# Kernel optimization log

Measured on AMD Instinct MI355X. Metric: run time of the kernel, lower is better.

Reference implementation:

```python
import jax, jax.numpy as jnp
import numpy as np

N = 163842   # icosahedron level-7 vertices
CH = 64
EPS = 1e-5
SLOPE = 0.2

def _bn_lrelu(x, g, b):
    # BatchNorm1d over vertex dim (training-mode batch stats, biased var) + LeakyReLU(0.2)
    mu = jnp.mean(x, axis=0)
    var = jnp.var(x, axis=0)
    y = (x - mu) * jax.lax.rsqrt(var + EPS) * g + b
    return jnp.where(y > 0, y, SLOPE * y)

def _onering_conv(x, neigh, W, bias):
    # gather 7 one-ring neighbors per vertex, flatten, linear project
    n = x.shape[0]
    feat = x[neigh].reshape(n, -1)          # [N, 7*C]
    return feat @ W + bias                  # [N, out]

def setup_inputs() -> dict:
    key = jax.random.key(0)
    ks = jax.random.split(key, 8)
    d = {
        "x": jax.random.normal(ks[0], (N, CH), jnp.float32),
        "neigh_orders": jax.random.randint(ks[1], (7 * N,), 0, N, jnp.int64),
    }
    for i, k in enumerate([1, 2, 3, 4]):
        cin = CH * k
        d[f"g{k}"] = jnp.ones((cin,), jnp.float32)
        d[f"b{k}"] = jnp.zeros((cin,), jnp.float32)
        d[f"W{k}"] = jax.random.normal(ks[2 + i], (7 * cin, CH), jnp.float32) * (1.0 / np.sqrt(7 * cin))
        d[f"wb{k}"] = jnp.zeros((CH,), jnp.float32)
    return d

def reference(x, neigh_orders, g1, b1, g2, b2, g3, b3, g4, b4,
              W1, wb1, W2, wb2, W3, wb3, W4, wb4):
    x1 = _onering_conv(_bn_lrelu(x, g1, b1), neigh_orders, W1, wb1)
    c2 = jnp.concatenate((x, x1), axis=1)
    x2 = _onering_conv(_bn_lrelu(c2, g2, b2), neigh_orders, W2, wb2)
    c3 = jnp.concatenate((x, x1, x2), axis=1)
    x3 = _onering_conv(_bn_lrelu(c3, g3, b3), neigh_orders, W3, wb3)
    c4 = jnp.concatenate((x, x1, x2, x3), axis=1)
    x4 = _onering_conv(_bn_lrelu(c4, g4, b4), neigh_orders, W4, wb4)
    return x4
```

## Files before the change

kernel.cpp:

```cpp
#include <hip/hip_runtime.h>
#include <stdint.h>

#define NV 163842
#define EPSV 1e-5f

using short8 = __attribute__((ext_vector_type(8))) short;
using f32x4  = __attribute__((ext_vector_type(4))) float;

static __device__ __forceinline__ unsigned short f2bf(float f) {
    union { float f; unsigned int i; } v; v.f = f;
    return (unsigned short)((v.i + 0x7FFFu + ((v.i >> 16) & 1u)) >> 16);
}
static __device__ __forceinline__ void bf2x(unsigned int w, float& a, float& b) {
    union { unsigned int i; float f; } lo, hi;
    lo.i = w << 16; hi.i = w & 0xFFFF0000u;
    a = lo.f; b = hi.f;
}
static __device__ __forceinline__ unsigned int pack2(float a, float b) {
    union { float f; unsigned int i; } ua, ub; ua.f = a; ub.f = b;
    return __builtin_amdgcn_perm(ub.i + 0x8000u, ua.i + 0x8000u, 0x07060302);
}

__global__ __launch_bounds__(256) void k_zero(float* __restrict__ ACC) {
    ACC[threadIdx.x] = 0.f;
    ACC[256 + threadIdx.x] = 0.f;
}

__global__ __launch_bounds__(256) void k_cast(const float* __restrict__ x,
                                              unsigned short* __restrict__ C,
                                              float* __restrict__ ACC) {
    const int t = threadIdx.x;
    const int wv = t >> 6, lane = t & 63;
    const int v = blockIdx.x * 64 + (t >> 2);
    const int c0 = (t & 3) * 16;
    float f[16];
    const bool valid = v < NV;
    if (valid) {
        const float4* p = (const float4*)(x + (size_t)v * 64 + c0);
#pragma unroll
        for (int i = 0; i < 4; ++i) {
            float4 q = p[i];
            f[i * 4 + 0] = q.x; f[i * 4 + 1] = q.y; f[i * 4 + 2] = q.z; f[i * 4 + 3] = q.w;
        }
        unsigned int o[8];
#pragma unroll
        for (int i = 0; i < 8; ++i)
            o[i] = ((unsigned int)f2bf(f[2 * i])) | (((unsigned int)f2bf(f[2 * i + 1])) << 16);
        uint4* dst = (uint4*)(C + (size_t)v * 256 + c0);
        dst[0] = uint4{o[0], o[1], o[2], o[3]};
        dst[1] = uint4{o[4], o[5], o[6], o[7]};
    } else {
#pragma unroll
        for (int i = 0; i < 16; ++i) f[i] = 0.f;
    }
    float s[16], s2[16];
#pragma unroll
    for (int i = 0; i < 16; ++i) { s[i] = f[i]; s2[i] = f[i] * f[i]; }
#pragma unroll
    for (int mask = 4; mask <= 32; mask <<= 1) {
#pragma unroll
        for (int i = 0; i < 16; ++i) {
            s[i]  += __shfl_xor(s[i],  mask);
            s2[i] += __shfl_xor(s2[i], mask);
        }
    }
    __shared__ float red[4 * 128];
    if ((lane >> 2) == 0) {
        int cb = (lane & 3) * 16;
#pragma unroll
        for (int i = 0; i < 16; ++i) {
            red[wv * 128 + cb + i]      = s[i];
            red[wv * 128 + 64 + cb + i] = s2[i];
        }
    }
    __syncthreads();
    if (t < 128) {
        float v4 = red[t] + red[128 + t] + red[256 + t] + red[384 + t];
        int c = t & 63, which = t >> 6;
        atomicAdd(&ACC[which * 256 + c], v4);
    }
}

__global__ __launch_bounds__(256) void k_wt_all(const float* __restrict__ W1,
                                                const float* __restrict__ W2,
                                                const float* __restrict__ W3,
                                                const float* __restrict__ W4,
                                                unsigned short* __restrict__ WT) {
    int j = blockIdx.x * 256 + threadIdx.x;
    if (j >= 286720) return;
    const float* W; int jj, K7;
    if (j < 28672)       { W = W1; jj = j;          K7 = 448;  }
    else if (j < 86016)  { W = W2; jj = j - 28672;  K7 = 896;  }
    else if (j < 172032) { W = W3; jj = j - 86016;  K7 = 1344; }
    else                 { W = W4; jj = j - 172032; K7 = 1792; }
    int n = jj / K7, k = jj - n * K7;
    WT[j] = f2bf(W[(size_t)k * 64 + n]);
}

template<int CIN, int GRP, bool FINAL>
__global__ __launch_bounds__(256) void k_gg(const unsigned short* __restrict__ C,
                                            const int* __restrict__ neigh,
                                            const unsigned short* __restrict__ WT,
                                            const float* __restrict__ g,
                                            const float* __restrict__ bglob,
                                            const float* __restrict__ wb,
                                            float* __restrict__ ACC,
                                            unsigned short* __restrict__ Cout,
                                            float* __restrict__ Fout) {
    constexpr int KB = CIN / 64;
    constexpr int NC = 7 * KB;
    constexpr int K7 = 7 * CIN;

    __shared__ float ssc[256], ssh[256];
    __shared__ int sIdx[896];
    __shared__ unsigned short sA[128 * 72];
    __shared__ unsigned short sW[64 * 72];

    const int t = threadIdx.x;
    const int v0 = blockIdx.x * 128;

    if (t < CIN) {
        float s = ACC[t], s2 = ACC[256 + t];
        float mu = s * (1.0f / NV);
        float var = fmaf(-mu, mu, s2 * (1.0f / NV));
        float sc = g[t] * rsqrtf(var + EPSV);
        ssc[t] = sc;
        ssh[t] = bglob[t] - mu * sc;
    }
    for (int q = t; q < 896; q += 256) {
        int gi = v0 * 7 + q;
        sIdx[q] = (gi < NV * 7) ? neigh[gi] : 0;
    }
    __syncthreads();

    const int wv = t >> 6, lane = t & 63;
    const int m = lane & 15, quad = lane >> 4;
    const int arow = t >> 1, ahalf = t & 1;
    const int wrow = t >> 2, wq = t & 3;

    f32x4 acc[2][4];
#pragma unroll
    for (int i = 0; i < 2; ++i)
#pragma unroll
        for (int j = 0; j < 4; ++j) acc[i][j] = f32x4{0.f, 0.f, 0.f, 0.f};

    auto load_chunk = [&](int c, uint4* aa, uint4& x0, uint4& x1) {
        int r = c / KB, kb = c - r * KB;
        int src = sIdx[arow * 7 + r];
        const uint4* pa = (const uint4*)(C + (size_t)src * 256 + kb * 64 + ahalf * 32);
        aa[0] = pa[0]; aa[1] = pa[1]; aa[2] = pa[2]; aa[3] = pa[3];
        const uint4* pw = (const uint4*)(WT + (size_t)wrow * K7 + c * 64 + wq * 16);
        x0 = pw[0]; x1 = pw[1];
    };
    auto stage = [&](const uint4* aa, uint4 x0, uint4 x1, int c) {
        int kb = c - (c / KB) * KB;
        int chb = kb * 64 + ahalf * 32;
        unsigned short* dstA = sA + arow * 72 + ahalf * 32;
#pragma unroll
        for (int i = 0; i < 4; ++i) {
            unsigned int u[4] = {aa[i].x, aa[i].y, aa[i].z, aa[i].w};
            unsigned int o[4];
#pragma unroll
            for (int jj = 0; jj < 4; ++jj) {
                float lo, hi; bf2x(u[jj], lo, hi);
                int ch = chb + i * 8 + jj * 2;
                float y0 = fmaf(lo, ssc[ch],     ssh[ch]);
                float y1 = fmaf(hi, ssc[ch + 1], ssh[ch + 1]);
                y0 = y0 > 0.f ? y0 : 0.2f * y0;
                y1 = y1 > 0.f ? y1 : 0.2f * y1;
                o[jj] = pack2(y0, y1);
            }
            *(uint4*)(dstA + i * 8) = uint4{o[0], o[1], o[2], o[3]};
        }
        *(uint4*)(sW + wrow * 72 + wq * 16)     = x0;
        *(uint4*)(sW + wrow * 72 + wq * 16 + 8) = x1;
    };

    uint4 a[4], w0, w1;
    load_chunk(0, a, w0, w1);
#pragma unroll 2
    for (int c = 0; c < NC; ++c) {
        uint4 na[4], nw0, nw1;
        if (c + 1 < NC) load_chunk(c + 1, na, nw0, nw1);
        stage(a, w0, w1, c);
        __syncthreads();
#pragma unroll
        for (int s = 0; s < 2; ++s) {
            short8 af0 = *(const short8*)(sA + (wv * 32 + m) * 72      + s * 32 + quad * 8);
            short8 af1 = *(const short8*)(sA + (wv * 32 + 16 + m) * 72 + s * 32 + quad * 8);
#pragma unroll
            for (int ct = 0; ct < 4; ++ct) {
                short8 bf = *(const short8*)(sW + (ct * 16 + m) * 72 + s * 32 + quad * 8);
                acc[0][ct] = __builtin_amdgcn_mfma_f32_16x16x32_bf16(af0, bf, acc[0][ct], 0, 0, 0);
                acc[1][ct] = __builtin_amdgcn_mfma_f32_16x16x32_bf16(af1, bf, acc[1][ct], 0, 0, 0);
            }
        }
        __syncthreads();
        if (c + 1 < NC) {
#pragma unroll
            for (int i = 0; i < 4; ++i) a[i] = na[i];
            w0 = nw0; w1 = nw1;
        }
    }

    float bsum[4]  = {0.f, 0.f, 0.f, 0.f};
    float b2sum[4] = {0.f, 0.f, 0.f, 0.f};
#pragma unroll
    for (int mt = 0; mt < 2; ++mt) {
#pragma unroll
        for (int ct = 0; ct < 4; ++ct) {
            int col = ct * 16 + m;
            float bv = wb[col];
#pragma unroll
            for (int j = 0; j < 4; ++j) {
                int vr = v0 + wv * 32 + mt * 16 + quad * 4 + j;
                float val = acc[mt][ct][j] + bv;
                if (vr < NV) {
                    if (FINAL) {
                        Fout[(size_t)vr * 64 + col] = val;
                    } else {
                        Cout[(size_t)vr * 256 + GRP * 64 + col] = f2bf(val);
                        bsum[ct] += val; b2sum[ct] += val * val;
                    }
                }
            }
        }
    }
    if (!FINAL) {
#pragma unroll
        for (int ct = 0; ct < 4; ++ct) {
            bsum[ct]  += __shfl_xor(bsum[ct], 16);
            bsum[ct]  += __shfl_xor(bsum[ct], 32);
            b2sum[ct] += __shfl_xor(b2sum[ct], 16);
            b2sum[ct] += __shfl_xor(b2sum[ct], 32);
        }
        float* red = (float*)sA;
        if (quad == 0) {
#pragma unroll
            for (int ct = 0; ct < 4; ++ct) {
                red[wv * 128 + ct * 16 + m]       = bsum[ct];
                red[512 + wv * 128 + ct * 16 + m] = b2sum[ct];
            }
        }
        __syncthreads();
        if (t < 128) {
            int c = t & 63, which = t >> 6;
            float v = red[which * 512 + c] + red[which * 512 + 128 + c] +
                      red[which * 512 + 256 + c] + red[which * 512 + 384 + c];
            atomicAdd(&ACC[which * 256 + GRP * 64 + c], v);
        }
    }
}

extern "C" void kernel_launch(void* const* d_in, const int* in_sizes, int n_in,
                              void* d_out, int out_size, void* d_ws, size_t ws_size,
                              hipStream_t stream) {
    const float* x     = (const float*)d_in[0];
    const int*   neigh = (const int*)d_in[1];
    const float* G[4]  = {(const float*)d_in[2],  (const float*)d_in[6],
                          (const float*)d_in[10], (const float*)d_in[14]};
    const float* B[4]  = {(const float*)d_in[3],  (const float*)d_in[7],
                          (const float*)d_in[11], (const float*)d_in[15]};
    const float* W[4]  = {(const float*)d_in[4],  (const float*)d_in[8],
                          (const float*)d_in[12], (const float*)d_in[16]};
    const float* WB[4] = {(const float*)d_in[5],  (const float*)d_in[9],
                          (const float*)d_in[13], (const float*)d_in[17]};
    float* out = (float*)d_out;

    char* ws = (char*)d_ws;
    size_t off = 0;
    unsigned short* C  = (unsigned short*)(ws + off); off += (size_t)NV * 256 * 2;
    unsigned short* WT = (unsigned short*)(ws + off); off += (size_t)286720 * 2;
    float* ACC         = (float*)(ws + off);          off += 512 * 4;

    k_zero<<<1, 256, 0, stream>>>(ACC);
    k_cast<<<(NV + 63) / 64, 256, 0, stream>>>(x, C, ACC);
    k_wt_all<<<(286720 + 255) / 256, 256, 0, stream>>>(W[0], W[1], W[2], W[3], WT);

    const int GG = (NV + 127) / 128;
    k_gg< 64, 1, false><<<GG, 256, 0, stream>>>(C, neigh, WT,          G[0], B[0], WB[0], ACC, C, nullptr);
    k_gg<128, 2, false><<<GG, 256, 0, stream>>>(C, neigh, WT + 28672,  G[1], B[1], WB[1], ACC, C, nullptr);
    k_gg<192, 3, false><<<GG, 256, 0, stream>>>(C, neigh, WT + 86016,  G[2], B[2], WB[2], ACC, C, nullptr);
    k_gg<256, 0, true ><<<GG, 256, 0, stream>>>(C, neigh, WT + 172032, G[3], B[3], WB[3], ACC, nullptr, out);
}
```

Before: 528.0 us.

## Precompute BN+LeakyReLU activations and gather MFMA operands directly from global

Moves the BN+LeakyReLU normalisation out of the gather-GEMM into a separate per-layer elementwise pass that writes a compact activation buffer. The GEMM kernel then loads A fragments straight from global memory into registers with a 3-deep prefetch, skipping the LDS staging of A. Weights are staged into LDS in large segments of 14 chunks, so there are far fewer barriers. Blocks grow to 512 threads covering 256 vertices. The cost is an extra full read and write of the activations per layer, plus uncoalesced 16-byte gathers per lane.

```diff
diff --git a/kernel.cpp b/kernel.cpp
--- a/kernel.cpp
+++ b/kernel.cpp
@@ -97,28 +97,14 @@
     WT[j] = f2bf(W[(size_t)k * 64 + n]);
 }
 
-template<int CIN, int GRP, bool FINAL>
-__global__ __launch_bounds__(256) void k_gg(const unsigned short* __restrict__ C,
-                                            const int* __restrict__ neigh,
-                                            const unsigned short* __restrict__ WT,
-                                            const float* __restrict__ g,
-                                            const float* __restrict__ bglob,
-                                            const float* __restrict__ wb,
-                                            float* __restrict__ ACC,
-                                            unsigned short* __restrict__ Cout,
-                                            float* __restrict__ Fout) {
-    constexpr int KB = CIN / 64;
-    constexpr int NC = 7 * KB;
-    constexpr int K7 = 7 * CIN;
-
-    __shared__ float ssc[256], ssh[256];
-    __shared__ int sIdx[896];
-    __shared__ unsigned short sA[128 * 72];
-    __shared__ unsigned short sW[64 * 72];
-
+template<int CIN>
+__global__ __launch_bounds__(256) void k_apply(const unsigned short* __restrict__ C,
+                                               const float* __restrict__ ACC,
+                                               const float* __restrict__ g,
+                                               const float* __restrict__ bglob,
+                                               unsigned short* __restrict__ Y) {
+    __shared__ float ssc[CIN], ssh[CIN];
     const int t = threadIdx.x;
-    const int v0 = blockIdx.x * 128;
-
     if (t < CIN) {
         float s = ACC[t], s2 = ACC[256 + t];
         float mu = s * (1.0f / NV);
@@ -127,7 +113,48 @@
         ssc[t] = sc;
         ssh[t] = bglob[t] - mu * sc;
     }
-    for (int q = t; q < 896; q += 256) {
+    __syncthreads();
+    constexpr int C8 = CIN / 8;
+    int e = blockIdx.x * 256 + t;
+    if (e >= NV * C8) return;
+    int v = e / C8, c8 = e - v * C8;
+    int ch = c8 * 8;
+    uint4 u = *(const uint4*)(C + (size_t)v * 256 + ch);
+    float f[8];
+    bf2x(u.x, f[0], f[1]); bf2x(u.y, f[2], f[3]);
+    bf2x(u.z, f[4], f[5]); bf2x(u.w, f[6], f[7]);
+    unsigned int o[4];
+#pragma unroll
+    for (int jj = 0; jj < 4; ++jj) {
+        float y0 = fmaf(f[2 * jj],     ssc[ch + 2 * jj],     ssh[ch + 2 * jj]);
+        float y1 = fmaf(f[2 * jj + 1], ssc[ch + 2 * jj + 1], ssh[ch + 2 * jj + 1]);
+        y0 = y0 > 0.f ? y0 : 0.2f * y0;
+        y1 = y1 > 0.f ? y1 : 0.2f * y1;
+        o[jj] = pack2(y0, y1);
+    }
+    *(uint4*)(Y + (size_t)v * CIN + ch) = uint4{o[0], o[1], o[2], o[3]};
+}
+
+template<int CIN, int GRP, bool FINAL>
+__global__ __launch_bounds__(512, 4) void k_gg(const unsigned short* __restrict__ Y,
+                                               const int* __restrict__ neigh,
+                                               const unsigned short* __restrict__ WT,
+                                               const float* __restrict__ wb,
+                                               float* __restrict__ ACC,
+                                               unsigned short* __restrict__ Cout,
+                                               float* __restrict__ Fout) {
+    constexpr int KB2 = CIN / 32;
+    constexpr int NC  = 7 * KB2;
+    constexpr int NSEG = NC / 14;
+    constexpr int K7  = 7 * CIN;
+
+    __shared__ int sIdx[1792];
+    __shared__ unsigned short sW[64 * 456];
+
+    const int t = threadIdx.x;
+    const int v0 = blockIdx.x * 256;
+
+    for (int q = t; q < 1792; q += 512) {
         int gi = v0 * 7 + q;
         sIdx[q] = (gi < NV * 7) ? neigh[gi] : 0;
     }
@@ -135,8 +162,15 @@
 
     const int wv = t >> 6, lane = t & 63;
     const int m = lane & 15, quad = lane >> 4;
-    const int arow = t >> 1, ahalf = t & 1;
-    const int wrow = t >> 2, wq = t & 3;
+    const int rb = wv * 32;
+    const int qoff = quad * 8;
+
+    int idx0[7], idx1[7];
+#pragma unroll
+    for (int r = 0; r < 7; ++r) {
+        idx0[r] = sIdx[(rb + m) * 7 + r];
+        idx1[r] = sIdx[(rb + 16 + m) * 7 + r];
+    }
 
     f32x4 acc[2][4];
 #pragma unroll
@@ -144,65 +178,50 @@
 #pragma unroll
         for (int j = 0; j < 4; ++j) acc[i][j] = f32x4{0.f, 0.f, 0.f, 0.f};
 
-    auto load_chunk = [&](int c, uint4* aa, uint4& x0, uint4& x1) {
-        int r = c / KB, kb = c - r * KB;
-        int src = sIdx[arow * 7 + r];
-        const uint4* pa = (const uint4*)(C + (size_t)src * 256 + kb * 64 + ahalf * 32);
-        aa[0] = pa[0]; aa[1] = pa[1]; aa[2] = pa[2]; aa[3] = pa[3];
-        const uint4* pw = (const uint4*)(WT + (size_t)wrow * K7 + c * 64 + wq * 16);
-        x0 = pw[0]; x1 = pw[1];
+    auto loadA = [&](int c, short8& A0, short8& A1) {
+        int r = c / KB2, kc = c - r * KB2;
+        int ko = kc * 32 + qoff;
+        A0 = *(const short8*)(Y + (size_t)idx0[r] * CIN + ko);
+        A1 = *(const short8*)(Y + (size_t)idx1[r] * CIN + ko);
     };
-    auto stage = [&](const uint4* aa, uint4 x0, uint4 x1, int c) {
-        int kb = c - (c / KB) * KB;
-        int chb = kb * 64 + ahalf * 32;
-        unsigned short* dstA = sA + arow * 72 + ahalf * 32;
-#pragma unroll
-        for (int i = 0; i < 4; ++i) {
-            unsigned int u[4] = {aa[i].x, aa[i].y, aa[i].z, aa[i].w};
-            unsigned int o[4];
-#pragma unroll
-            for (int jj = 0; jj < 4; ++jj) {
-                float lo, hi; bf2x(u[jj], lo, hi);
-                int ch = chb + i * 8 + jj * 2;
-                float y0 = fmaf(lo, ssc[ch],     ssh[ch]);
-                float y1 = fmaf(hi, ssc[ch + 1], ssh[ch + 1]);
-                y0 = y0 > 0.f ? y0 : 0.2f * y0;
-                y1 = y1 > 0.f ? y1 : 0.2f * y1;
-                o[jj] = pack2(y0, y1);
+
+    short8 a0[3], a1[3];
+    loadA(0, a0[0], a1[0]);
+    loadA(1, a0[1], a1[1]);
+    loadA(2, a0[2], a1[2]);
+
+#pragma unroll
+    for (int seg = 0; seg < NSEG; ++seg) {
+        __syncthreads();
+        {
+            const int n = wv * 8 + (lane >> 3);
+            const int ch0 = lane & 7;
+            const unsigned short* src = WT + (size_t)n * K7 + seg * 448;
+            unsigned short* dst = sW + n * 456;
+#pragma unroll
+            for (int p = 0; p < 7; ++p) {
+                int ch16 = p * 8 + ch0;
+                *(uint4*)(dst + ch16 * 8) = *(const uint4*)(src + ch16 * 8);
             }
-            *(uint4*)(dstA + i * 8) = uint4{o[0], o[1], o[2], o[3]};
-        }
-        *(uint4*)(sW + wrow * 72 + wq * 16)     = x0;
-        *(uint4*)(sW + wrow * 72 + wq * 16 + 8) = x1;
-    };
-
-    uint4 a[4], w0, w1;
-    load_chunk(0, a, w0, w1);
-#pragma unroll 2
-    for (int c = 0; c < NC; ++c) {
-        uint4 na[4], nw0, nw1;
-        if (c + 1 < NC) load_chunk(c + 1, na, nw0, nw1);
-        stage(a, w0, w1, c);
+        }
         __syncthreads();
 #pragma unroll
-        for (int s = 0; s < 2; ++s) {
-            short8 af0 = *(const short8*)(sA + (wv * 32 + m) * 72      + s * 32 + quad * 8);
-            short8 af1 = *(const short8*)(sA + (wv * 32 + 16 + m) * 72 + s * 32 + quad * 8);
+        for (int cc = 0; cc < 14; ++cc) {
+            const int c = seg * 14 + cc;
+            short8 na0, na1;
+            if (c + 3 < NC) loadA(c + 3, na0, na1);
+            const int buf = c % 3;
 #pragma unroll
             for (int ct = 0; ct < 4; ++ct) {
-                short8 bf = *(const short8*)(sW + (ct * 16 + m) * 72 + s * 32 + quad * 8);
-                acc[0][ct] = __builtin_amdgcn_mfma_f32_16x16x32_bf16(af0, bf, acc[0][ct], 0, 0, 0);
-                acc[1][ct] = __builtin_amdgcn_mfma_f32_16x16x32_bf16(af1, bf, acc[1][ct], 0, 0, 0);
+                short8 bf = *(const short8*)(sW + (ct * 16 + m) * 456 + cc * 32 + qoff);
+                acc[0][ct] = __builtin_amdgcn_mfma_f32_16x16x32_bf16(a0[buf], bf, acc[0][ct], 0, 0, 0);
+                acc[1][ct] = __builtin_amdgcn_mfma_f32_16x16x32_bf16(a1[buf], bf, acc[1][ct], 0, 0, 0);
             }
-        }
-        __syncthreads();
-        if (c + 1 < NC) {
-#pragma unroll
-            for (int i = 0; i < 4; ++i) a[i] = na[i];
-            w0 = nw0; w1 = nw1;
-        }
-    }
-
+            if (c + 3 < NC) { a0[buf] = na0; a1[buf] = na1; }
+        }
+    }
+
+    __syncthreads();
     float bsum[4]  = {0.f, 0.f, 0.f, 0.f};
     float b2sum[4] = {0.f, 0.f, 0.f, 0.f};
 #pragma unroll
@@ -234,20 +253,21 @@
             b2sum[ct] += __shfl_xor(b2sum[ct], 16);
             b2sum[ct] += __shfl_xor(b2sum[ct], 32);
         }
-        float* red = (float*)sA;
+        float* red = (float*)sW;
         if (quad == 0) {
 #pragma unroll
             for (int ct = 0; ct < 4; ++ct) {
-                red[wv * 128 + ct * 16 + m]       = bsum[ct];
-                red[512 + wv * 128 + ct * 16 + m] = b2sum[ct];
+                red[wv * 128 + ct * 16 + m]        = bsum[ct];
+                red[1024 + wv * 128 + ct * 16 + m] = b2sum[ct];
             }
         }
         __syncthreads();
         if (t < 128) {
             int c = t & 63, which = t >> 6;
-            float v = red[which * 512 + c] + red[which * 512 + 128 + c] +
-                      red[which * 512 + 256 + c] + red[which * 512 + 384 + c];
-            atomicAdd(&ACC[which * 256 + GRP * 64 + c], v);
+            float s = 0.f;
+#pragma unroll
+            for (int w = 0; w < 8; ++w) s += red[which * 1024 + w * 128 + c];
+            atomicAdd(&ACC[which * 256 + GRP * 64 + c], s);
         }
     }
 }
@@ -270,6 +290,7 @@
     char* ws = (char*)d_ws;
     size_t off = 0;
     unsigned short* C  = (unsigned short*)(ws + off); off += (size_t)NV * 256 * 2;
+    unsigned short* Yb = (unsigned short*)(ws + off); off += (size_t)NV * 256 * 2;
     unsigned short* WT = (unsigned short*)(ws + off); off += (size_t)286720 * 2;
     float* ACC         = (float*)(ws + off);          off += 512 * 4;
 
@@ -277,9 +298,15 @@
     k_cast<<<(NV + 63) / 64, 256, 0, stream>>>(x, C, ACC);
     k_wt_all<<<(286720 + 255) / 256, 256, 0, stream>>>(W[0], W[1], W[2], W[3], WT);
 
-    const int GG = (NV + 127) / 128;
-    k_gg< 64, 1, false><<<GG, 256, 0, stream>>>(C, neigh, WT,          G[0], B[0], WB[0], ACC, C, nullptr);
-    k_gg<128, 2, false><<<GG, 256, 0, stream>>>(C, neigh, WT + 28672,  G[1], B[1], WB[1], ACC, C, nullptr);
-    k_gg<192, 3, false><<<GG, 256, 0, stream>>>(C, neigh, WT + 86016,  G[2], B[2], WB[2], ACC, C, nullptr);
-    k_gg<256, 0, true ><<<GG, 256, 0, stream>>>(C, neigh, WT + 172032, G[3], B[3], WB[3], ACC, nullptr, out);
-}
+    const int GG = (NV + 255) / 256;
+#define APPLY(CIN, LI) k_apply<CIN><<<((NV * (CIN / 8)) + 255) / 256, 256, 0, stream>>>(C, ACC, G[LI], B[LI], Yb)
+    APPLY(64, 0);
+    k_gg< 64, 1, false><<<GG, 512, 0, stream>>>(Yb, neigh, WT,          WB[0], ACC, C, nullptr);
+    APPLY(128, 1);
+    k_gg<128, 2, false><<<GG, 512, 0, stream>>>(Yb, neigh, WT + 28672,  WB[1], ACC, C, nullptr);
+    APPLY(192, 2);
+    k_gg<192, 3, false><<<GG, 512, 0, stream>>>(Yb, neigh, WT + 86016,  WB[2], ACC, C, nullptr);
+    APPLY(256, 3);
+    k_gg<256, 0, true ><<<GG, 512, 0, stream>>>(Yb, neigh, WT + 172032, WB[3], ACC, nullptr, out);
+#undef APPLY
+}
```

After: 561.7 us. +6.4%, slower.

## Load gathered A fragments directly into registers and stage weights per segment

Applied to the files above, without the earlier changes.

Removes the shared-memory staging of the gathered, normalized activations. Each lane now gathers its own MFMA A-fragment from global memory using precomputed neighbor offsets and applies BN+LeakyReLU in registers. Weights are copied to LDS in larger 224-wide segments, so there are fewer barriers, and a 3-deep register prefetch ping-pongs across segments. The BN scale and shift are packed as bf16 pairs in LDS, which costs precision. Occupancy is hinted with launch_bounds(256,4).

```diff
diff --git a/kernel.cpp b/kernel.cpp
--- a/kernel.cpp
+++ b/kernel.cpp
@@ -98,23 +98,23 @@
 }
 
 template<int CIN, int GRP, bool FINAL>
-__global__ __launch_bounds__(256) void k_gg(const unsigned short* __restrict__ C,
-                                            const int* __restrict__ neigh,
-                                            const unsigned short* __restrict__ WT,
-                                            const float* __restrict__ g,
-                                            const float* __restrict__ bglob,
-                                            const float* __restrict__ wb,
-                                            float* __restrict__ ACC,
-                                            unsigned short* __restrict__ Cout,
-                                            float* __restrict__ Fout) {
-    constexpr int KB = CIN / 64;
-    constexpr int NC = 7 * KB;
-    constexpr int K7 = 7 * CIN;
-
-    __shared__ float ssc[256], ssh[256];
+__global__ __launch_bounds__(256, 4) void k_gg(const unsigned short* __restrict__ C,
+                                               const int* __restrict__ neigh,
+                                               const unsigned short* __restrict__ WT,
+                                               const float* __restrict__ g,
+                                               const float* __restrict__ bglob,
+                                               const float* __restrict__ wb,
+                                               float* __restrict__ ACC,
+                                               unsigned short* __restrict__ Cout,
+                                               float* __restrict__ Fout) {
+    constexpr int KB2  = CIN / 32;
+    constexpr int NC   = 7 * KB2;
+    constexpr int K7   = 7 * CIN;
+    constexpr int NSEG = K7 / 224;
+
+    __shared__ unsigned int sBN[256];
     __shared__ int sIdx[896];
-    __shared__ unsigned short sA[128 * 72];
-    __shared__ unsigned short sW[64 * 72];
+    __shared__ unsigned short sW[64 * 232];
 
     const int t = threadIdx.x;
     const int v0 = blockIdx.x * 128;
@@ -124,8 +124,8 @@
         float mu = s * (1.0f / NV);
         float var = fmaf(-mu, mu, s2 * (1.0f / NV));
         float sc = g[t] * rsqrtf(var + EPSV);
-        ssc[t] = sc;
-        ssh[t] = bglob[t] - mu * sc;
+        float sh = bglob[t] - mu * sc;
+        sBN[t] = pack2(sc, sh);
     }
     for (int q = t; q < 896; q += 256) {
         int gi = v0 * 7 + q;
@@ -135,8 +135,14 @@
 
     const int wv = t >> 6, lane = t & 63;
     const int m = lane & 15, quad = lane >> 4;
-    const int arow = t >> 1, ahalf = t & 1;
-    const int wrow = t >> 2, wq = t & 3;
+
+    unsigned int voff0[7], voff1[7];
+#pragma unroll
+    for (int r = 0; r < 7; ++r) {
+        voff0[r] = (unsigned)sIdx[(wv * 32 + m) * 7 + r] * 512u + (unsigned)quad * 16u;
+        voff1[r] = (unsigned)sIdx[(wv * 32 + 16 + m) * 7 + r] * 512u + (unsigned)quad * 16u;
+    }
+    const char* Cb = (const char*)C;
 
     f32x4 acc[2][4];
 #pragma unroll
@@ -144,65 +150,84 @@
 #pragma unroll
         for (int j = 0; j < 4; ++j) acc[i][j] = f32x4{0.f, 0.f, 0.f, 0.f};
 
-    auto load_chunk = [&](int c, uint4* aa, uint4& x0, uint4& x1) {
-        int r = c / KB, kb = c - r * KB;
-        int src = sIdx[arow * 7 + r];
-        const uint4* pa = (const uint4*)(C + (size_t)src * 256 + kb * 64 + ahalf * 32);
-        aa[0] = pa[0]; aa[1] = pa[1]; aa[2] = pa[2]; aa[3] = pa[3];
-        const uint4* pw = (const uint4*)(WT + (size_t)wrow * K7 + c * 64 + wq * 16);
-        x0 = pw[0]; x1 = pw[1];
+    auto loadRaw = [&](int c, uint4& p0, uint4& p1) {
+        int r = c / KB2, kc = c % KB2;
+        p0 = *(const uint4*)(Cb + voff0[r] + kc * 64);
+        p1 = *(const uint4*)(Cb + voff1[r] + kc * 64);
     };
-    auto stage = [&](const uint4* aa, uint4 x0, uint4 x1, int c) {
-        int kb = c - (c / KB) * KB;
-        int chb = kb * 64 + ahalf * 32;
-        unsigned short* dstA = sA + arow * 72 + ahalf * 32;
-#pragma unroll
-        for (int i = 0; i < 4; ++i) {
-            unsigned int u[4] = {aa[i].x, aa[i].y, aa[i].z, aa[i].w};
-            unsigned int o[4];
-#pragma unroll
-            for (int jj = 0; jj < 4; ++jj) {
-                float lo, hi; bf2x(u[jj], lo, hi);
-                int ch = chb + i * 8 + jj * 2;
-                float y0 = fmaf(lo, ssc[ch],     ssh[ch]);
-                float y1 = fmaf(hi, ssc[ch + 1], ssh[ch + 1]);
-                y0 = y0 > 0.f ? y0 : 0.2f * y0;
-                y1 = y1 > 0.f ? y1 : 0.2f * y1;
-                o[jj] = pack2(y0, y1);
+    auto bnA = [&](const uint4& p0, const uint4& p1, int c, short8& A0, short8& A1) {
+        int kc = c % KB2;
+        int chb = kc * 32 + quad * 8;
+        uint4 q0 = *(const uint4*)&sBN[chb];
+        uint4 q1 = *(const uint4*)&sBN[chb + 4];
+        float sc[8], sh[8];
+        bf2x(q0.x, sc[0], sh[0]); bf2x(q0.y, sc[1], sh[1]);
+        bf2x(q0.z, sc[2], sh[2]); bf2x(q0.w, sc[3], sh[3]);
+        bf2x(q1.x, sc[4], sh[4]); bf2x(q1.y, sc[5], sh[5]);
+        bf2x(q1.z, sc[6], sh[6]); bf2x(q1.w, sc[7], sh[7]);
+        unsigned int u0[4] = {p0.x, p0.y, p0.z, p0.w};
+        unsigned int u1[4] = {p1.x, p1.y, p1.z, p1.w};
+        unsigned int o0[4], o1[4];
+#pragma unroll
+        for (int d = 0; d < 4; ++d) {
+            float a, b, y0, y1;
+            bf2x(u0[d], a, b);
+            y0 = fmaf(a, sc[2 * d], sh[2 * d]);     y0 = fmaxf(y0, 0.2f * y0);
+            y1 = fmaf(b, sc[2 * d + 1], sh[2 * d + 1]); y1 = fmaxf(y1, 0.2f * y1);
+            o0[d] = pack2(y0, y1);
+            bf2x(u1[d], a, b);
+            y0 = fmaf(a, sc[2 * d], sh[2 * d]);     y0 = fmaxf(y0, 0.2f * y0);
+            y1 = fmaf(b, sc[2 * d + 1], sh[2 * d + 1]); y1 = fmaxf(y1, 0.2f * y1);
+            o1[d] = pack2(y0, y1);
+        }
+        union { uint4 u; short8 s; } c0, c1;
+        c0.u = uint4{o0[0], o0[1], o0[2], o0[3]};
+        c1.u = uint4{o1[0], o1[1], o1[2], o1[3]};
+        A0 = c0.s; A1 = c1.s;
+    };
+
+    uint4 pa0[3], pa1[3], qa0[3], qa1[3];
+
+    auto run_seg = [&](int seg, uint4 (&ca0)[3], uint4 (&ca1)[3],
+                       uint4 (&na0)[3], uint4 (&na1)[3]) {
+        __syncthreads();
+        {
+            const int n = t >> 2, qq = t & 3;
+            const unsigned short* src = WT + (size_t)n * K7 + seg * 224 + qq * 56;
+            unsigned short* dst = sW + n * 232 + qq * 56;
+#pragma unroll
+            for (int p = 0; p < 7; ++p)
+                *(uint4*)(dst + p * 8) = *(const uint4*)(src + p * 8);
+        }
+        if (seg + 1 < NSEG) {
+#pragma unroll
+            for (int d = 0; d < 3; ++d)
+                loadRaw((seg + 1) * 7 + d, na0[d], na1[d]);
+        }
+        __syncthreads();
+#pragma unroll
+        for (int cc = 0; cc < 7; ++cc) {
+            const int c = seg * 7 + cc;
+            short8 A0, A1;
+            bnA(ca0[cc % 3], ca1[cc % 3], c, A0, A1);
+            if (cc < 4) loadRaw(c + 3, ca0[cc % 3], ca1[cc % 3]);
+#pragma unroll
+            for (int ct = 0; ct < 4; ++ct) {
+                short8 bf = *(const short8*)(sW + (ct * 16 + m) * 232 + cc * 32 + quad * 8);
+                acc[0][ct] = __builtin_amdgcn_mfma_f32_16x16x32_bf16(A0, bf, acc[0][ct], 0, 0, 0);
+                acc[1][ct] = __builtin_amdgcn_mfma_f32_16x16x32_bf16(A1, bf, acc[1][ct], 0, 0, 0);
             }
-            *(uint4*)(dstA + i * 8) = uint4{o[0], o[1], o[2], o[3]};
-        }
-        *(uint4*)(sW + wrow * 72 + wq * 16)     = x0;
-        *(uint4*)(sW + wrow * 72 + wq * 16 + 8) = x1;
+        }
     };
 
-    uint4 a[4], w0, w1;
-    load_chunk(0, a, w0, w1);
-#pragma unroll 2
-    for (int c = 0; c < NC; ++c) {
-        uint4 na[4], nw0, nw1;
-        if (c + 1 < NC) load_chunk(c + 1, na, nw0, nw1);
-        stage(a, w0, w1, c);
-        __syncthreads();
-#pragma unroll
-        for (int s = 0; s < 2; ++s) {
-            short8 af0 = *(const short8*)(sA + (wv * 32 + m) * 72      + s * 32 + quad * 8);
-            short8 af1 = *(const short8*)(sA + (wv * 32 + 16 + m) * 72 + s * 32 + quad * 8);
-#pragma unroll
-            for (int ct = 0; ct < 4; ++ct) {
-                short8 bf = *(const short8*)(sW + (ct * 16 + m) * 72 + s * 32 + quad * 8);
-                acc[0][ct] = __builtin_amdgcn_mfma_f32_16x16x32_bf16(af0, bf, acc[0][ct], 0, 0, 0);
-                acc[1][ct] = __builtin_amdgcn_mfma_f32_16x16x32_bf16(af1, bf, acc[1][ct], 0, 0, 0);
-            }
-        }
-        __syncthreads();
-        if (c + 1 < NC) {
-#pragma unroll
-            for (int i = 0; i < 4; ++i) a[i] = na[i];
-            w0 = nw0; w1 = nw1;
-        }
-    }
-
+#pragma unroll
+    for (int d = 0; d < 3; ++d) loadRaw(d, pa0[d], pa1[d]);
+    for (int seg = 0; seg < NSEG; ++seg) {
+        if (seg & 1) run_seg(seg, qa0, qa1, pa0, pa1);
+        else         run_seg(seg, pa0, pa1, qa0, qa1);
+    }
+
+    __syncthreads();
     float bsum[4]  = {0.f, 0.f, 0.f, 0.f};
     float b2sum[4] = {0.f, 0.f, 0.f, 0.f};
 #pragma unroll
@@ -234,7 +259,7 @@
             b2sum[ct] += __shfl_xor(b2sum[ct], 16);
             b2sum[ct] += __shfl_xor(b2sum[ct], 32);
         }
-        float* red = (float*)sA;
+        float* red = (float*)sW;
         if (quad == 0) {
 #pragma unroll
             for (int ct = 0; ct < 4; ++ct) {
@@ -245,9 +270,9 @@
         __syncthreads();
         if (t < 128) {
             int c = t & 63, which = t >> 6;
-            float v = red[which * 512 + c] + red[which * 512 + 128 + c] +
+            float s = red[which * 512 + c] + red[which * 512 + 128 + c] +
                       red[which * 512 + 256 + c] + red[which * 512 + 384 + c];
-            atomicAdd(&ACC[which * 256 + GRP * 64 + c], v);
+            atomicAdd(&ACC[which * 256 + GRP * 64 + c], s);
         }
     }
 }
```

Result: slower. 1.943 ms (+268.0%).

## Reorder one-ring conv as per-vertex linear then neighbor gather-sum

Applied to the files above, without the earlier changes.

Each layer is split into two kernels. The first computes, for every vertex, its BN+LeakyReLU features times each of the 7 weight slices (Z = act @ W_r, stored as bf16). The second gathers and sums the 7 projected 64-channel rows of each vertex's neighbors, adding the bias and accumulating BN statistics. Gathering 64-channel bf16 rows instead of CIN-wide rows cuts the random gather traffic, and BN is applied once per vertex rather than once per gathered neighbor. The cost is an extra intermediate buffer of up to N*448 bf16, extra rounding of partial sums to bf16, and a fallback two-pass path with a float partial buffer when the workspace is too small.

```diff
diff --git a/kernel.cpp b/kernel.cpp
--- a/kernel.cpp
+++ b/kernel.cpp
@@ -97,158 +97,199 @@
     WT[j] = f2bf(W[(size_t)k * 64 + n]);
 }
 
-template<int CIN, int GRP, bool FINAL>
-__global__ __launch_bounds__(256) void k_gg(const unsigned short* __restrict__ C,
-                                            const int* __restrict__ neigh,
-                                            const unsigned short* __restrict__ WT,
-                                            const float* __restrict__ g,
-                                            const float* __restrict__ bglob,
-                                            const float* __restrict__ wb,
-                                            float* __restrict__ ACC,
-                                            unsigned short* __restrict__ Cout,
-                                            float* __restrict__ Fout) {
-    constexpr int KB = CIN / 64;
-    constexpr int NC = 7 * KB;
+template<int CIN>
+__global__ __launch_bounds__(512, 4) void k_lin(const unsigned short* __restrict__ C,
+                                                const unsigned short* __restrict__ WT,
+                                                const float* __restrict__ g,
+                                                const float* __restrict__ bglob,
+                                                const float* __restrict__ ACC,
+                                                unsigned short* __restrict__ Z,
+                                                int ZW, int r0, int r1) {
     constexpr int K7 = 7 * CIN;
-
-    __shared__ float ssc[256], ssh[256];
-    __shared__ int sIdx[896];
-    __shared__ unsigned short sA[128 * 72];
-    __shared__ unsigned short sW[64 * 72];
+    constexpr int KC = CIN / 32;
+    constexpr int LW = CIN + 8;
+    constexpr int C8 = CIN / 8;
+    __shared__ unsigned int sBN[CIN];
+    __shared__ unsigned short sW[64 * LW];
 
     const int t = threadIdx.x;
-    const int v0 = blockIdx.x * 128;
-
     if (t < CIN) {
         float s = ACC[t], s2 = ACC[256 + t];
         float mu = s * (1.0f / NV);
         float var = fmaf(-mu, mu, s2 * (1.0f / NV));
         float sc = g[t] * rsqrtf(var + EPSV);
-        ssc[t] = sc;
-        ssh[t] = bglob[t] - mu * sc;
-    }
-    for (int q = t; q < 896; q += 256) {
+        sBN[t] = pack2(sc, bglob[t] - mu * sc);
+    }
+    const int wv = t >> 6, lane = t & 63, m = lane & 15, quad = lane >> 4;
+    int vA = blockIdx.x * 128 + wv * 16 + m;
+    if (vA >= NV) vA = NV - 1;
+    const unsigned short* Arow = C + (size_t)vA * 256 + quad * 8;
+
+    uint4 raw[KC];
+#pragma unroll
+    for (int kc = 0; kc < KC; ++kc) raw[kc] = *(const uint4*)(Arow + kc * 32);
+    __syncthreads();
+
+    short8 afr[KC];
+#pragma unroll
+    for (int kc = 0; kc < KC; ++kc) {
+        int chb = kc * 32 + quad * 8;
+        uint4 q0 = *(const uint4*)&sBN[chb];
+        uint4 q1 = *(const uint4*)&sBN[chb + 4];
+        unsigned int qs[8] = {q0.x, q0.y, q0.z, q0.w, q1.x, q1.y, q1.z, q1.w};
+        unsigned int u[4]  = {raw[kc].x, raw[kc].y, raw[kc].z, raw[kc].w};
+        unsigned int o[4];
+#pragma unroll
+        for (int d = 0; d < 4; ++d) {
+            float sc0, sh0, sc1, sh1, a, b;
+            bf2x(qs[2 * d], sc0, sh0);
+            bf2x(qs[2 * d + 1], sc1, sh1);
+            bf2x(u[d], a, b);
+            float y0 = fmaf(a, sc0, sh0); y0 = fmaxf(y0, 0.2f * y0);
+            float y1 = fmaf(b, sc1, sh1); y1 = fmaxf(y1, 0.2f * y1);
+            o[d] = pack2(y0, y1);
+        }
+        union { uint4 uu; short8 ss; } cv;
+        cv.uu = uint4{o[0], o[1], o[2], o[3]};
+        afr[kc] = cv.ss;
+    }
+
+    const int vOutB = blockIdx.x * 128 + wv * 16 + quad * 4;
+    for (int r = r0; r < r1; ++r) {
+        for (int e = t; e < 64 * C8; e += 512) {
+            int n = e / C8, k8 = e - n * C8;
+            *(uint4*)(sW + n * LW + k8 * 8) =
+                *(const uint4*)(WT + (size_t)n * K7 + r * CIN + k8 * 8);
+        }
+        __syncthreads();
+        f32x4 acc[4];
+#pragma unroll
+        for (int i = 0; i < 4; ++i) acc[i] = f32x4{0.f, 0.f, 0.f, 0.f};
+#pragma unroll
+        for (int kc = 0; kc < KC; ++kc) {
+#pragma unroll
+            for (int ct = 0; ct < 4; ++ct) {
+                short8 bf = *(const short8*)(sW + (ct * 16 + m) * LW + kc * 32 + quad * 8);
+                acc[ct] = __builtin_amdgcn_mfma_f32_16x16x32_bf16(afr[kc], bf, acc[ct], 0, 0, 0);
+            }
+        }
+        unsigned short* zr = Z + (size_t)(r - r0) * 64;
+#pragma unroll
+        for (int ct = 0; ct < 4; ++ct)
+#pragma unroll
+            for (int j = 0; j < 4; ++j) {
+                int v = vOutB + j;
+                if (v < NV) zr[(size_t)v * ZW + ct * 16 + m] = f2bf(acc[ct][j]);
+            }
+        __syncthreads();
+    }
+}
+
+template<int R0, int R1, bool FINAL, bool RDP, bool WRP>
+__global__ __launch_bounds__(512) void k_gath(const unsigned short* __restrict__ Z, int ZW,
+                                              const int* __restrict__ neigh,
+                                              const float* __restrict__ wb,
+                                              float* __restrict__ ACC,
+                                              unsigned short* __restrict__ CoutG,
+                                              float* __restrict__ Fout,
+                                              float* __restrict__ PART,
+                                              int GRP) {
+    __shared__ int sIdx[448];
+    __shared__ float red[1024];
+    const int t = threadIdx.x;
+    const int v0 = blockIdx.x * 64;
+    for (int q = t; q < 448; q += 512) {
         int gi = v0 * 7 + q;
         sIdx[q] = (gi < NV * 7) ? neigh[gi] : 0;
     }
     __syncthreads();
-
+    const int vloc = t >> 3, c8 = t & 7;
+    const int v = v0 + vloc;
+    const bool ok = v < NV;
+
+    float a[8];
+    if (RDP) {
+        float4 p0{0, 0, 0, 0}, p1{0, 0, 0, 0};
+        if (ok) {
+            p0 = *(const float4*)(PART + (size_t)v * 64 + c8 * 8);
+            p1 = *(const float4*)(PART + (size_t)v * 64 + c8 * 8 + 4);
+        }
+        a[0] = p0.x; a[1] = p0.y; a[2] = p0.z; a[3] = p0.w;
+        a[4] = p1.x; a[5] = p1.y; a[6] = p1.z; a[7] = p1.w;
+    } else {
+#pragma unroll
+        for (int i = 0; i < 8; ++i) a[i] = 0.f;
+    }
+
+    uint4 zr[R1 - R0];
+#pragma unroll
+    for (int r = R0; r < R1; ++r) {
+        int u = sIdx[vloc * 7 + r];
+        zr[r - R0] = *(const uint4*)(Z + (size_t)u * ZW + (size_t)(r - R0) * 64 + c8 * 8);
+    }
+#pragma unroll
+    for (int r = 0; r < R1 - R0; ++r) {
+        float x0, x1;
+        bf2x(zr[r].x, x0, x1); a[0] += x0; a[1] += x1;
+        bf2x(zr[r].y, x0, x1); a[2] += x0; a[3] += x1;
+        bf2x(zr[r].z, x0, x1); a[4] += x0; a[5] += x1;
+        bf2x(zr[r].w, x0, x1); a[6] += x0; a[7] += x1;
+    }
+
+    if (WRP) {
+        if (ok) {
+            *(float4*)(PART + (size_t)v * 64 + c8 * 8)     = float4{a[0], a[1], a[2], a[3]};
+            *(float4*)(PART + (size_t)v * 64 + c8 * 8 + 4) = float4{a[4], a[5], a[6], a[7]};
+        }
+        return;
+    }
+#pragma unroll
+    for (int i = 0; i < 8; ++i) a[i] += wb[c8 * 8 + i];
+
+    if (FINAL) {
+        if (ok) {
+            *(float4*)(Fout + (size_t)v * 64 + c8 * 8)     = float4{a[0], a[1], a[2], a[3]};
+            *(float4*)(Fout + (size_t)v * 64 + c8 * 8 + 4) = float4{a[4], a[5], a[6], a[7]};
+        }
+        return;
+    }
+    unsigned int o[4];
+#pragma unroll
+    for (int i = 0; i < 4; ++i) o[i] = pack2(a[2 * i], a[2 * i + 1]);
+    if (ok) *(uint4*)(CoutG + (size_t)v * 256 + c8 * 8) = uint4{o[0], o[1], o[2], o[3]};
+
+    float s[8], s2[8];
+#pragma unroll
+    for (int i = 0; i < 8; ++i) {
+        float vv = ok ? a[i] : 0.f;
+        s[i] = vv; s2[i] = vv * vv;
+    }
+#pragma unroll
+    for (int mask = 8; mask <= 32; mask <<= 1) {
+#pragma unroll
+        for (int i = 0; i < 8; ++i) {
+            s[i]  += __shfl_xor(s[i],  mask);
+            s2[i] += __shfl_xor(s2[i], mask);
+        }
+    }
     const int wv = t >> 6, lane = t & 63;
-    const int m = lane & 15, quad = lane >> 4;
-    const int arow = t >> 1, ahalf = t & 1;
-    const int wrow = t >> 2, wq = t & 3;
-
-    f32x4 acc[2][4];
-#pragma unroll
-    for (int i = 0; i < 2; ++i)
-#pragma unroll
-        for (int j = 0; j < 4; ++j) acc[i][j] = f32x4{0.f, 0.f, 0.f, 0.f};
-
-    auto load_chunk = [&](int c, uint4* aa, uint4& x0, uint4& x1) {
-        int r = c / KB, kb = c - r * KB;
-        int src = sIdx[arow * 7 + r];
-        const uint4* pa = (const uint4*)(C + (size_t)src * 256 + kb * 64 + ahalf * 32);
-        aa[0] = pa[0]; aa[1] = pa[1]; aa[2] = pa[2]; aa[3] = pa[3];
-        const uint4* pw = (const uint4*)(WT + (size_t)wrow * K7 + c * 64 + wq * 16);
-        x0 = pw[0]; x1 = pw[1];
-    };
-    auto stage = [&](const uint4* aa, uint4 x0, uint4 x1, int c) {
-        int kb = c - (c / KB) * KB;
-        int chb = kb * 64 + ahalf * 32;
-        unsigned short* dstA = sA + arow * 72 + ahalf * 32;
-#pragma unroll
-        for (int i = 0; i < 4; ++i) {
-            unsigned int u[4] = {aa[i].x, aa[i].y, aa[i].z, aa[i].w};
-            unsigned int o[4];
-#pragma unroll
-            for (int jj = 0; jj < 4; ++jj) {
-                float lo, hi; bf2x(u[jj], lo, hi);
-                int ch = chb + i * 8 + jj * 2;
-                float y0 = fmaf(lo, ssc[ch],     ssh[ch]);
-                float y1 = fmaf(hi, ssc[ch + 1], ssh[ch + 1]);
-                y0 = y0 > 0.f ? y0 : 0.2f * y0;
-                y1 = y1 > 0.f ? y1 : 0.2f * y1;
-                o[jj] = pack2(y0, y1);
-            }
-            *(uint4*)(dstA + i * 8) = uint4{o[0], o[1], o[2], o[3]};
-        }
-        *(uint4*)(sW + wrow * 72 + wq * 16)     = x0;
-        *(uint4*)(sW + wrow * 72 + wq * 16 + 8) = x1;
-    };
-
-    uint4 a[4], w0, w1;
-    load_chunk(0, a, w0, w1);
-#pragma unroll 2
-    for (int c = 0; c < NC; ++c) {
-        uint4 na[4], nw0, nw1;
-        if (c + 1 < NC) load_chunk(c + 1, na, nw0, nw1);
-        stage(a, w0, w1, c);
-        __syncthreads();
-#pragma unroll
-        for (int s = 0; s < 2; ++s) {
-            short8 af0 = *(const short8*)(sA + (wv * 32 + m) * 72      + s * 32 + quad * 8);
-            short8 af1 = *(const short8*)(sA + (wv * 32 + 16 + m) * 72 + s * 32 + quad * 8);
-#pragma unroll
-            for (int ct = 0; ct < 4; ++ct) {
-                short8 bf = *(const short8*)(sW + (ct * 16 + m) * 72 + s * 32 + quad * 8);
-                acc[0][ct] = __builtin_amdgcn_mfma_f32_16x16x32_bf16(af0, bf, acc[0][ct], 0, 0, 0);
-                acc[1][ct] = __builtin_amdgcn_mfma_f32_16x16x32_bf16(af1, bf, acc[1][ct], 0, 0, 0);
-            }
-        }
-        __syncthreads();
-        if (c + 1 < NC) {
-#pragma unroll
-            for (int i = 0; i < 4; ++i) a[i] = na[i];
-            w0 = nw0; w1 = nw1;
-        }
-    }
-
-    float bsum[4]  = {0.f, 0.f, 0.f, 0.f};
-    float b2sum[4] = {0.f, 0.f, 0.f, 0.f};
-#pragma unroll
-    for (int mt = 0; mt < 2; ++mt) {
-#pragma unroll
-        for (int ct = 0; ct < 4; ++ct) {
-            int col = ct * 16 + m;
-            float bv = wb[col];
-#pragma unroll
-            for (int j = 0; j < 4; ++j) {
-                int vr = v0 + wv * 32 + mt * 16 + quad * 4 + j;
-                float val = acc[mt][ct][j] + bv;
-                if (vr < NV) {
-                    if (FINAL) {
-                        Fout[(size_t)vr * 64 + col] = val;
-                    } else {
-                        Cout[(size_t)vr * 256 + GRP * 64 + col] = f2bf(val);
-                        bsum[ct] += val; b2sum[ct] += val * val;
-                    }
-                }
-            }
-        }
-    }
-    if (!FINAL) {
-#pragma unroll
-        for (int ct = 0; ct < 4; ++ct) {
-            bsum[ct]  += __shfl_xor(bsum[ct], 16);
-            bsum[ct]  += __shfl_xor(bsum[ct], 32);
-            b2sum[ct] += __shfl_xor(b2sum[ct], 16);
-            b2sum[ct] += __shfl_xor(b2sum[ct], 32);
-        }
-        float* red = (float*)sA;
-        if (quad == 0) {
-#pragma unroll
-            for (int ct = 0; ct < 4; ++ct) {
-                red[wv * 128 + ct * 16 + m]       = bsum[ct];
-                red[512 + wv * 128 + ct * 16 + m] = b2sum[ct];
-            }
-        }
-        __syncthreads();
-        if (t < 128) {
-            int c = t & 63, which = t >> 6;
-            float v = red[which * 512 + c] + red[which * 512 + 128 + c] +
-                      red[which * 512 + 256 + c] + red[which * 512 + 384 + c];
-            atomicAdd(&ACC[which * 256 + GRP * 64 + c], v);
-        }
+    if ((lane >> 3) == 0) {
+#pragma unroll
+        for (int i = 0; i < 8; ++i) {
+            red[wv * 64 + c8 * 8 + i]       = s[i];
+            red[512 + wv * 64 + c8 * 8 + i] = s2[i];
+        }
+    }
+    __syncthreads();
+    if (t < 64) {
+        float ss = 0.f, ss2 = 0.f;
+#pragma unroll
+        for (int w = 0; w < 8; ++w) {
+            ss  += red[w * 64 + t];
+            ss2 += red[512 + w * 64 + t];
+        }
+        atomicAdd(&ACC[GRP * 64 + t], ss);
+        atomicAdd(&ACC[256 + GRP * 64 + t], ss2);
     }
 }
 
@@ -272,14 +313,47 @@
     unsigned short* C  = (unsigned short*)(ws + off); off += (size_t)NV * 256 * 2;
     unsigned short* WT = (unsigned short*)(ws + off); off += (size_t)286720 * 2;
     float* ACC         = (float*)(ws + off);          off += 512 * 4;
+    unsigned short* Z  = (unsigned short*)(ws + off);
+    const size_t zFull = (size_t)NV * 448 * 2;
+    const bool full = ws_size >= off + zFull;
 
     k_zero<<<1, 256, 0, stream>>>(ACC);
     k_cast<<<(NV + 63) / 64, 256, 0, stream>>>(x, C, ACC);
     k_wt_all<<<(286720 + 255) / 256, 256, 0, stream>>>(W[0], W[1], W[2], W[3], WT);
 
-    const int GG = (NV + 127) / 128;
-    k_gg< 64, 1, false><<<GG, 256, 0, stream>>>(C, neigh, WT,          G[0], B[0], WB[0], ACC, C, nullptr);
-    k_gg<128, 2, false><<<GG, 256, 0, stream>>>(C, neigh, WT + 28672,  G[1], B[1], WB[1], ACC, C, nullptr);
-    k_gg<192, 3, false><<<GG, 256, 0, stream>>>(C, neigh, WT + 86016,  G[2], B[2], WB[2], ACC, C, nullptr);
-    k_gg<256, 0, true ><<<GG, 256, 0, stream>>>(C, neigh, WT + 172032, G[3], B[3], WB[3], ACC, nullptr, out);
-}
+    const int GL = (NV + 127) / 128;
+    const int GH = (NV + 63) / 64;
+    const int WOFF[4] = {0, 28672, 86016, 172032};
+
+    if (full) {
+#define LAYER(CIN, LI, GRP)                                                              \
+        k_lin<CIN><<<GL, 512, 0, stream>>>(C, WT + WOFF[LI], G[LI], B[LI], ACC, Z, 448, 0, 7); \
+        k_gath<0, 7, false, false, false><<<GH, 512, 0, stream>>>(                       \
+            Z, 448, neigh, WB[LI], ACC, C + GRP * 64, nullptr, nullptr, GRP)
+        LAYER(64, 0, 1);
+        LAYER(128, 1, 2);
+        LAYER(192, 2, 3);
+#undef LAYER
+        k_lin<256><<<GL, 512, 0, stream>>>(C, WT + WOFF[3], G[3], B[3], ACC, Z, 448, 0, 7);
+        k_gath<0, 7, true, false, false><<<GH, 512, 0, stream>>>(
+            Z, 448, neigh, WB[3], ACC, nullptr, out, nullptr, 0);
+    } else {
+#define LAYER(CIN, LI, GRP)                                                              \
+        k_lin<CIN><<<GL, 512, 0, stream>>>(C, WT + WOFF[LI], G[LI], B[LI], ACC, Z, 256, 0, 4); \
+        k_gath<0, 4, false, false, true><<<GH, 512, 0, stream>>>(                        \
+            Z, 256, neigh, WB[LI], ACC, nullptr, nullptr, out, GRP);                     \
+        k_lin<CIN><<<GL, 512, 0, stream>>>(C, WT + WOFF[LI], G[LI], B[LI], ACC, Z, 192, 4, 7); \
+        k_gath<4, 7, false, true, false><<<GH, 512, 0, stream>>>(                        \
+            Z, 192, neigh, WB[LI], ACC, C + GRP * 64, nullptr, out, GRP)
+        LAYER(64, 0, 1);
+        LAYER(128, 1, 2);
+        LAYER(192, 2, 3);
+#undef LAYER
+        k_lin<256><<<GL, 512, 0, stream>>>(C, WT + WOFF[3], G[3], B[3], ACC, Z, 256, 0, 4);
+        k_gath<0, 4, false, false, true><<<GH, 512, 0, stream>>>(
+            Z, 256, neigh, WB[3], ACC, nullptr, nullptr, out, 0);
+        k_lin<256><<<GL, 512, 0, stream>>>(C, WT + WOFF[3], G[3], B[3], ACC, Z, 192, 4, 7);
+        k_gath<4, 7, true, true, false><<<GH, 512, 0, stream>>>(
+            Z, 192, neigh, WB[3], ACC, nullptr, out, out, 0);
+    }
+}
```

After: 619.8 us. 17.4% more time.
